# Kernel tuning notes

Measured on AMD Instinct MI355X. Metric: run time of the kernel, lower is better.

The kernel has to match this reference:

```python
import jax, jax.numpy as jnp
import numpy as np

NUM_BINS = 5
TAIL = 1.0
MIN_BIN_W = 1e-3
MIN_BIN_H = 1e-3


def conv2d(x, w, b, pad):
    y = jax.lax.conv_general_dilated(x, w, (1, 1), [(pad, pad), (pad, pad)],
                                     dimension_numbers=("NCHW", "OIHW", "NCHW"))
    return y + b[None, :, None, None]


def transform_net(x, w1, b1, w2, b2, w3, b3):
    h = jax.nn.relu(conv2d(x, w1, b1, 1))
    h = jax.nn.relu(conv2d(h, w2, b2, 0))
    return conv2d(h, w3, b3, 1)


def _pad_last_left(a):
    return jnp.pad(a, [(0, 0)] * (a.ndim - 1) + [(1, 0)])


def quadratic_spline(x, uw, uh):
    # nflows quadratic_spline with left=bottom=-TAIL, right=top=TAIL
    inputs = (x + TAIL) / (2.0 * TAIL)  # rescale to [0,1]
    widths = jax.nn.softmax(uw, axis=-1)
    widths = MIN_BIN_W + (1.0 - MIN_BIN_W * NUM_BINS) * widths
    uh_exp = jnp.exp(uh)  # [..., NUM_BINS-1]
    first_w = 0.5 * widths[..., 0]
    last_w = 0.5 * widths[..., -1]
    numerator = (0.5 * first_w * uh_exp[..., 0] + 0.5 * last_w * uh_exp[..., -1]
                 + jnp.sum(0.5 * (uh_exp[..., :-1] + uh_exp[..., 1:]) * widths[..., 1:-1], axis=-1))
    constant = numerator / (1.0 - 0.5 * first_w - 0.5 * last_w)
    uh_exp = jnp.concatenate([constant[..., None], uh_exp, constant[..., None]], axis=-1)  # NUM_BINS+1 knot heights
    area = jnp.sum(0.5 * (uh_exp[..., :-1] + uh_exp[..., 1:]) * widths, axis=-1, keepdims=True)
    heights = uh_exp / area
    heights = MIN_BIN_H + (1.0 - MIN_BIN_H) * heights
    bin_cdf = jnp.cumsum(0.5 * (heights[..., :-1] + heights[..., 1:]) * widths, axis=-1)
    bin_cdf = _pad_last_left(bin_cdf.at[..., -1].set(1.0))  # [..., NUM_BINS+1]
    bin_loc = jnp.cumsum(widths, axis=-1)
    bin_loc = _pad_last_left(bin_loc.at[..., -1].set(1.0))  # [..., NUM_BINS+1]
    # searchsorted: bin index per element
    idx = jnp.clip(jnp.sum((inputs[..., None] >= bin_loc).astype(jnp.int32), axis=-1) - 1, 0, NUM_BINS - 1)
    take = lambda t, i: jnp.take_along_axis(t, i[..., None], axis=-1)[..., 0]
    loc = take(bin_loc, idx)
    cdf = take(bin_cdf, idx)
    h_l = take(heights, idx)
    h_r = take(heights, idx + 1)
    w = take(widths, idx)
    alpha = (inputs - loc) / w
    a = 0.5 * (h_r - h_l) * w
    b = h_l * w
    out = jnp.clip(a * alpha * alpha + b * alpha + cdf, 0.0, 1.0)
    lad = jnp.log(alpha * (h_r - h_l) + h_l)  # log(top-bottom)-log(right-left)=0
    out = out * (2.0 * TAIL) - TAIL
    return out, lad


def unconstrained_quadratic_spline(x, uw, uh):
    inside = (x >= -TAIL) & (x <= TAIL)
    xc = jnp.clip(x, -TAIL, TAIL)
    s_out, s_lad = quadratic_spline(xc, uw, uh)
    out = jnp.where(inside, s_out, x)  # linear tails
    lad = jnp.where(inside, s_lad, 0.0)
    return out, lad


def setup_inputs() -> dict:
    key = jax.random.key(0)
    ks = jax.random.split(key, 8)
    B, C, H, W = 32, 12, 128, 128
    hid = 128
    c_half = C // 2
    c_out = c_half * (2 * NUM_BINS - 1)  # 54
    s = 0.05
    return {
        "x": jax.random.normal(ks[0], (B, C, H, W), dtype=jnp.float32),
        "objective": jnp.zeros((B,), dtype=jnp.float32),
        "w1": s * jax.random.normal(ks[1], (hid, c_half, 3, 3), dtype=jnp.float32),
        "b1": jnp.zeros((hid,), dtype=jnp.float32),
        "w2": s * jax.random.normal(ks[2], (hid, hid, 1, 1), dtype=jnp.float32),
        "b2": jnp.zeros((hid,), dtype=jnp.float32),
        "w3": s * jax.random.normal(ks[3], (c_out, hid, 3, 3), dtype=jnp.float32),
        "b3": jnp.zeros((c_out,), dtype=jnp.float32),
    }


def reference(x, objective, w1, b1, w2, b2, w3, b3):
    identity_split, transform_split = jnp.split(x, 2, axis=1)
    params = transform_net(identity_split, w1, b1, w2, b2, w3, b3)  # [B, c/2*(2K-1), H, W]
    b, c, h, w = transform_split.shape
    params = params.reshape(b, c, -1, h, w).transpose(0, 1, 3, 4, 2)  # [B,c,H,W,2K-1]
    uw = params[..., :NUM_BINS]
    uh = params[..., NUM_BINS:]
    transformed, lad = unconstrained_quadratic_spline(transform_split, uw, uh)
    output = jnp.concatenate([identity_split, transformed], axis=1)
    objective = objective + jnp.sum(lad, axis=(1, 2, 3))
    return output, objective
```

## Files before the change

### kernel.cpp

```cpp
#include <hip/hip_runtime.h>
#include <hip/hip_bf16.h>
#include <math.h>

#define B 32
#define CFULL 12
#define CH 6
#define HH 128
#define WW 128
#define HID 128
#define CO3 54
#define NB 5
#define OUT_ELEMS (B*CFULL*HH*WW)
#define H2_BYTES (size_t)(B*HH*WW*HID*2)
#define WFRAG_ELEMS (9*4*4*64*8)
#define W1F_ELEMS (2*8*64*8)
#define W2F_ELEMS (4*8*64*8)

typedef __bf16 bf16x8 __attribute__((ext_vector_type(8)));
typedef float f32x4 __attribute__((ext_vector_type(4)));

__device__ __forceinline__ ushort f2bf(float f) {
    uint b = __float_as_uint(f);
    uint r = (b + 0x7FFFu + ((b >> 16) & 1u)) >> 16;
    return (ushort)r;
}

union UBF { uint4 u; bf16x8 b; };

__global__ __launch_bounds__(256) void k_prep_all(
    const float* __restrict__ w1, const float* __restrict__ w2, const float* __restrict__ w3,
    const float* __restrict__ obj_in, float* __restrict__ obj_out,
    ushort* __restrict__ W1f, ushort* __restrict__ W2f, ushort* __restrict__ W3f)
{
    int idx = blockIdx.x * 256 + threadIdx.x;
    if (blockIdx.x == 0 && threadIdx.x < B) obj_out[threadIdx.x] = obj_in[threadIdx.x];

    if (idx < WFRAG_ELEMS) {
        int j    = idx & 7;
        int lane = (idx >> 3) & 63;
        int nf   = (idx >> 9) & 3;
        int kb   = (idx >> 11) & 3;
        int t    = idx >> 13;
        int co = nf * 16 + (lane & 15);
        int ci = kb * 32 + 8 * (lane >> 4) + j;
        float v = (co < CO3) ? w3[(co * HID + ci) * 9 + t] : 0.f;
        W3f[idx] = f2bf(v);
    } else if (idx < WFRAG_ELEMS + W1F_ELEMS) {
        int i1 = idx - WFRAG_ELEMS;
        int j = i1 & 7, lane = (i1 >> 3) & 63, nf = (i1 >> 9) & 7, ks = i1 >> 12;
        int co = nf * 16 + (lane & 15);
        int k  = ks * 32 + (lane >> 4) * 8 + j;
        W1f[i1] = f2bf(k < 54 ? w1[co * 54 + k] : 0.f);
    } else if (idx < WFRAG_ELEMS + W1F_ELEMS + W2F_ELEMS) {
        int i2 = idx - WFRAG_ELEMS - W1F_ELEMS;
        int j = i2 & 7, lane = (i2 >> 3) & 63, nf = (i2 >> 9) & 7, ks = (i2 >> 12) & 3;
        int co = nf * 16 + (lane & 15);
        int ci = ks * 32 + (lane >> 4) * 8 + j;
        W2f[i2] = f2bf(w2[co * 128 + ci]);
    }
}

__global__ __launch_bounds__(256) void k_conv12(
    const float* __restrict__ x,
    const ushort* __restrict__ W1f, const float* __restrict__ b1,
    const ushort* __restrict__ W2f, const float* __restrict__ b2,
    ushort* __restrict__ h2)
{
    __shared__ char buf[32768];

    ushort* xs = (ushort*)buf;
    char* Albase = buf + 4864;
    char* h1 = buf;
    char* h2st = buf;

    const int b = blockIdx.x >> 7;
    const int h = blockIdx.x & 127;
    const int tid = threadIdx.x;
    const int lane = tid & 63;
    const int wv = tid >> 6;
    const int lr = lane & 15;
    const int kg = lane >> 4;

    for (int i = tid; i < 6*3*130; i += 256) {
        int ci = i / 390; int rem = i - ci*390;
        int r = rem / 130; int xw = rem - r*130;
        int hh = h + r - 1, ww = xw - 1;
        float v = 0.f;
        if (hh >= 0 && hh < HH && ww >= 0 && ww < WW)
            v = x[((b*CFULL + ci)*HH + hh)*WW + ww];
        xs[(ci*3 + r)*132 + xw] = f2bf(v);
    }
    __syncthreads();

    for (int it = 0; it < 4; ++it) {
        int item = (it << 8) + tid;
        int px = item & 127;
        int g  = item >> 7;
        uint pk[4];
#pragma unroll
        for (int jj = 0; jj < 4; ++jj) {
            int k0 = g*8 + jj*2;
            int k1 = k0 + 1;
            uint v0 = 0, v1 = 0;
            if (k0 < 54) { int ci = k0/9; int rem = k0 - ci*9; int r = rem/3; int dx = rem - r*3;
                           v0 = xs[(ci*3 + r)*132 + px + dx]; }
            if (k1 < 54) { int ci = k1/9; int rem = k1 - ci*9; int r = rem/3; int dx = rem - r*3;
                           v1 = xs[(ci*3 + r)*132 + px + dx]; }
            pk[jj] = v0 | (v1 << 16);
        }
        uint4 q; q.x = pk[0]; q.y = pk[1]; q.z = pk[2]; q.w = pk[3];
        *(uint4*)(Albase + px*128 + ((g << 4) ^ (((px >> 1) & 7) << 4))) = q;
    }
    __syncthreads();

    f32x4 acc[2][8];
#pragma unroll
    for (int mm = 0; mm < 2; ++mm)
#pragma unroll
        for (int nf = 0; nf < 8; ++nf) acc[mm][nf] = (f32x4){0.f,0.f,0.f,0.f};

    const int px0 = wv*32 + lr;
    const int px1 = px0 + 16;
#pragma unroll
    for (int ks = 0; ks < 2; ++ks) {
        UBF a0, a1;
        a0.u = *(const uint4*)(Albase + px0*128 + ((ks*64 + kg*16) ^ (((px0 >> 1) & 7) << 4)));
        a1.u = *(const uint4*)(Albase + px1*128 + ((ks*64 + kg*16) ^ (((px1 >> 1) & 7) << 4)));
        const char* wp = (const char*)W1f + ks*8192 + lane*16;
#pragma unroll
        for (int nf = 0; nf < 8; ++nf) {
            UBF bf; bf.u = *(const uint4*)(wp + nf*1024);
            acc[0][nf] = __builtin_amdgcn_mfma_f32_16x16x32_bf16(a0.b, bf.b, acc[0][nf], 0, 0, 0);
            acc[1][nf] = __builtin_amdgcn_mfma_f32_16x16x32_bf16(a1.b, bf.b, acc[1][nf], 0, 0, 0);
        }
    }
    __syncthreads();

    float b1v[8];
#pragma unroll
    for (int nf = 0; nf < 8; ++nf) b1v[nf] = b1[nf*16 + lr];
#pragma unroll
    for (int mm = 0; mm < 2; ++mm)
#pragma unroll
        for (int nf = 0; nf < 8; ++nf) {
            int co2 = (nf*16 + lr) * 2;
#pragma unroll
            for (int rg = 0; rg < 4; ++rg) {
                int px = wv*32 + mm*16 + kg*4 + rg;
                float v = fmaxf(acc[mm][nf][rg] + b1v[nf], 0.f);
                *(ushort*)(h1 + px*256 + (co2 ^ (((px >> 1) & 7) << 4))) = f2bf(v);
            }
        }
    __syncthreads();

#pragma unroll
    for (int mm = 0; mm < 2; ++mm)
#pragma unroll
        for (int nf = 0; nf < 8; ++nf) acc[mm][nf] = (f32x4){0.f,0.f,0.f,0.f};
#pragma unroll
    for (int ks = 0; ks < 4; ++ks) {
        UBF a0, a1;
        a0.u = *(const uint4*)(h1 + px0*256 + ((ks*64 + kg*16) ^ (((px0 >> 1) & 7) << 4)));
        a1.u = *(const uint4*)(h1 + px1*256 + ((ks*64 + kg*16) ^ (((px1 >> 1) & 7) << 4)));
        const char* wp = (const char*)W2f + ks*8192 + lane*16;
#pragma unroll
        for (int nf = 0; nf < 8; ++nf) {
            UBF bf; bf.u = *(const uint4*)(wp + nf*1024);
            acc[0][nf] = __builtin_amdgcn_mfma_f32_16x16x32_bf16(a0.b, bf.b, acc[0][nf], 0, 0, 0);
            acc[1][nf] = __builtin_amdgcn_mfma_f32_16x16x32_bf16(a1.b, bf.b, acc[1][nf], 0, 0, 0);
        }
    }
    __syncthreads();

    float b2v[8];
#pragma unroll
    for (int nf = 0; nf < 8; ++nf) b2v[nf] = b2[nf*16 + lr];
#pragma unroll
    for (int mm = 0; mm < 2; ++mm)
#pragma unroll
        for (int nf = 0; nf < 8; ++nf) {
            int co2 = (nf*16 + lr) * 2;
#pragma unroll
            for (int rg = 0; rg < 4; ++rg) {
                int px = wv*32 + mm*16 + kg*4 + rg;
                float v = fmaxf(acc[mm][nf][rg] + b2v[nf], 0.f);
                *(ushort*)(h2st + px*256 + (co2 ^ (((px >> 1) & 7) << 4))) = f2bf(v);
            }
        }
    __syncthreads();

    const size_t outbase = (size_t)((b*HH + h)*WW) * HID;
    for (int c = tid; c < 2048; c += 256) {
        int px = c >> 4; int cb = (c & 15) << 4;
        uint4 v = *(const uint4*)(h2st + px*256 + (cb ^ (((px >> 1) & 7) << 4)));
        *(uint4*)&h2[outbase + (size_t)c*8] = v;
    }
}

__global__ __launch_bounds__(256, 3) void k_conv3_spline(
    const float* __restrict__ x,
    const ushort* __restrict__ h2,
    const ushort* __restrict__ Wfrag, const float* __restrict__ b3,
    float* __restrict__ out, float* __restrict__ obj)
{
    __shared__ char xsb[33792];
    __shared__ float red[4];

    const int g = blockIdx.x;
    const int b = blockIdx.y;
    const int tid = threadIdx.x;
    const int px = tid & 127;
    const int t7 = (tid >> 7) & 1;

    float xr0, xr1, xr2, xr3, xr4, xr5;
    {
        size_t base;
#define PRO(RR, KS, DST) \
        base = ((size_t)(b*CFULL + (t7 + 2*(KS)))*HH + (2*g + (RR)))*WW + px; \
        out[base] = x[base]; \
        DST = x[base + (size_t)CH*HH*WW];
        PRO(0,0,xr0) PRO(0,1,xr1) PRO(0,2,xr2)
        PRO(1,0,xr3) PRO(1,1,xr4) PRO(1,2,xr5)
#undef PRO
    }

    const int lane = tid & 63;
    const int wv   = tid >> 6;
    const int mrow = wv >> 1;
    const int ncol = wv & 1;
    const int kg   = lane >> 4;
    const int lr   = lane & 15;

    f32x4 acc[8][2];
#pragma unroll
    for (int mf = 0; mf < 8; ++mf) {
        acc[mf][0] = (f32x4){0.f,0.f,0.f,0.f};
        acc[mf][1] = (f32x4){0.f,0.f,0.f,0.f};
    }

    const char* wbase = (const char*)Wfrag + ncol*2048 + lane*16;

#pragma unroll 1
    for (int q = 0; q < 4; ++q) {
        if (q) __syncthreads();

        for (int i = tid; i < 2080; i += 256) {
            int r = i / 520; int rem = i - r*520;
            int wl = rem >> 2; int c4 = rem & 3;
            int hh = 2*g - 1 + r, ww = wl - 1;
            uint4 v = {0,0,0,0};
            if (hh >= 0 && hh < HH && ww >= 0 && ww < WW)
                v = *(const uint4*)&h2[(size_t)((b*HH + hh)*WW + ww)*HID + q*32 + c4*8];
            *(uint4*)(xsb + r*8448 + wl*64 + ((c4*16) ^ (((wl >> 1) & 3) << 4))) = v;
        }
        __syncthreads();

#pragma unroll 1
        for (int r3 = 0; r3 < 3; ++r3) {
            const char* rowb = xsb + (mrow + r3)*8448;
#pragma unroll
            for (int dx = 0; dx < 3; ++dx) {
                const int t = r3*3 + dx;
                const char* wp = wbase + (((t << 2) + q) << 12);
                UBF b0; b0.u = *(const uint4*)(wp);
                UBF b1; b1.u = *(const uint4*)(wp + 1024);
#pragma unroll
                for (int mf = 0; mf < 8; ++mf) {
                    const int wl = mf*16 + lr + dx;
                    UBF a; a.u = *(const uint4*)(rowb + wl*64 + ((kg*16) ^ (((wl >> 1) & 3) << 4)));
                    acc[mf][0] = __builtin_amdgcn_mfma_f32_16x16x32_bf16(a.b, b0.b, acc[mf][0], 0, 0, 0);
                    acc[mf][1] = __builtin_amdgcn_mfma_f32_16x16x32_bf16(a.b, b1.b, acc[mf][1], 0, 0, 0);
                }
            }
        }
    }
    __syncthreads();

    float* pl = (float*)xsb;
    float lad = 0.f;

#pragma unroll
    for (int r = 0; r < 2; ++r) {
        if (r) __syncthreads();

        if (mrow == r) {
#pragma unroll
            for (int mf = 0; mf < 8; ++mf)
#pragma unroll
                for (int nf = 0; nf < 2; ++nf) {
                    const int co = ncol*32 + nf*16 + lr;
                    const int p0 = mf*16 + (kg << 2);
                    *(f32x4*)&pl[co*132 + p0] = acc[mf][nf];
                }
        }
        __syncthreads();

#pragma unroll
        for (int ks = 0; ks < 3; ++ks) {
            const int c = __builtin_amdgcn_readfirstlane(t7 + 2*ks);
            const float xraw = (r == 0) ? (ks == 0 ? xr0 : ks == 1 ? xr1 : xr2)
                                        : (ks == 0 ? xr3 : ks == 1 ? xr4 : xr5);

            float u[9];
#pragma unroll
            for (int j = 0; j < 9; ++j) u[j] = pl[(c*9 + j)*132 + px] + b3[c*9 + j];

            bool inside = (xraw >= -1.f) && (xraw <= 1.f);
            float xc = fminf(fmaxf(xraw, -1.f), 1.f);
            float in01 = (xc + 1.f) * 0.5f;

            float m = u[0];
#pragma unroll
            for (int i2 = 1; i2 < 5; ++i2) m = fmaxf(m, u[i2]);
            float e[5], es = 0.f;
#pragma unroll
            for (int i2 = 0; i2 < 5; ++i2) { e[i2] = expf(u[i2] - m); es += e[i2]; }
            float wdt[5];
#pragma unroll
            for (int i2 = 0; i2 < 5; ++i2) wdt[i2] = 0.001f + (1.f - 0.001f*NB) * (e[i2] / es);

            float eh[4];
#pragma unroll
            for (int i2 = 0; i2 < 4; ++i2) eh[i2] = expf(u[5 + i2]);

            float first_w = 0.5f * wdt[0], last_w = 0.5f * wdt[4];
            float numer = 0.5f*first_w*eh[0] + 0.5f*last_w*eh[3]
                        + 0.5f*(eh[0]+eh[1])*wdt[1]
                        + 0.5f*(eh[1]+eh[2])*wdt[2]
                        + 0.5f*(eh[2]+eh[3])*wdt[3];
            float cst = numer / (1.f - 0.5f*first_w - 0.5f*last_w);

            float kn[6] = {cst, eh[0], eh[1], eh[2], eh[3], cst};
            float area = 0.f;
#pragma unroll
            for (int i2 = 0; i2 < 5; ++i2) area += 0.5f*(kn[i2]+kn[i2+1])*wdt[i2];
            float hts[6];
#pragma unroll
            for (int i2 = 0; i2 < 6; ++i2) hts[i2] = 0.001f + (1.f - 0.001f) * (kn[i2] / area);

            float C[6]; C[0] = 0.f;
#pragma unroll
            for (int i2 = 0; i2 < 5; ++i2) C[i2+1] = C[i2] + 0.5f*(hts[i2]+hts[i2+1])*wdt[i2];
            C[5] = 1.f;
            float L[6]; L[0] = 0.f;
#pragma unroll
            for (int i2 = 0; i2 < 5; ++i2) L[i2+1] = L[i2] + wdt[i2];
            L[5] = 1.f;

            int idx = 0;
#pragma unroll
            for (int i2 = 1; i2 < 6; ++i2) idx += (in01 >= L[i2]) ? 1 : 0;
            idx = min(idx, 4);

            float loc = L[0], cdf = C[0], hl = hts[0], hr = hts[1], wb2 = wdt[0];
#pragma unroll
            for (int i2 = 1; i2 < 5; ++i2) {
                if (i2 == idx) { loc = L[i2]; cdf = C[i2]; hl = hts[i2]; hr = hts[i2+1]; wb2 = wdt[i2]; }
            }

            float alpha = (in01 - loc) / wb2;
            float aa = 0.5f*(hr - hl)*wb2;
            float bb = hl*wb2;
            float o = fminf(fmaxf(aa*alpha*alpha + bb*alpha + cdf, 0.f), 1.f);
            float sl = logf(alpha*(hr - hl) + hl);
            float outv = o*2.f - 1.f;
            if (!inside) { outv = xraw; sl = 0.f; }
            out[((size_t)(b*CFULL + CH + c)*HH + (2*g + r))*WW + px] = outv;
            lad += sl;
        }
    }

#pragma unroll
    for (int off = 32; off > 0; off >>= 1) lad += __shfl_down(lad, off, 64);
    if ((tid & 63) == 0) red[tid >> 6] = lad;
    __syncthreads();
    if (tid == 0) {
        float s = red[0] + red[1] + red[2] + red[3];
        atomicAdd(&obj[b], s);
    }
}

extern "C" void kernel_launch(void* const* d_in, const int* in_sizes, int n_in,
                              void* d_out, int out_size, void* d_ws, size_t ws_size,
                              hipStream_t stream) {
    const float* x   = (const float*)d_in[0];
    const float* obj = (const float*)d_in[1];
    const float* w1  = (const float*)d_in[2];
    const float* b1  = (const float*)d_in[3];
    const float* w2  = (const float*)d_in[4];
    const float* b2  = (const float*)d_in[5];
    const float* w3  = (const float*)d_in[6];
    const float* b3  = (const float*)d_in[7];

    float* out_t = (float*)d_out;
    float* obj_o = out_t + OUT_ELEMS;
    ushort* h2  = (ushort*)d_ws;
    ushort* W3f = (ushort*)((char*)d_ws + H2_BYTES);
    ushort* W1f = (ushort*)((char*)d_ws + H2_BYTES + 147456);
    ushort* W2f = (ushort*)((char*)d_ws + H2_BYTES + 147456 + 16384);

    const int prep_items = WFRAG_ELEMS + W1F_ELEMS + W2F_ELEMS;
    k_prep_all<<<(prep_items + 255)/256, 256, 0, stream>>>(w1, w2, w3, obj, obj_o, W1f, W2f, W3f);
    k_conv12<<<B*HH, 256, 0, stream>>>(x, W1f, b1, W2f, b2, h2);
    k_conv3_spline<<<dim3(HH/2, B), 256, 0, stream>>>(x, h2, W3f, b3, out_t, obj_o);
}
```

Measured before the change: 278.1 us.

## Prefetch next conv3 channel slab into registers and vectorize conv1/conv2 epilogue stores

In the conv3+spline kernel, the global loads of the next 32-channel h2 slab are issued into registers before the MFMA loop over the current slab and written to LDS afterwards, so global latency overlaps with compute. In the conv1/conv2 kernel, the MFMA operands are swapped so each lane holds four consecutive output channels for one pixel. The epilogue then packs them into a single 8-byte LDS store with a float4 bias load, replacing four scalar 2-byte stores. The prefetch costs 9 uint4 registers per thread (36 VGPRs), which may pressure occupancy under launch_bounds(256,3).

New measurement: 391.1 us. +40.6%, slower.

```diff
diff --git a/kernel.cpp b/kernel.cpp
--- a/kernel.cpp
+++ b/kernel.cpp
@@ -23,6 +23,9 @@
     uint b = __float_as_uint(f);
     uint r = (b + 0x7FFFu + ((b >> 16) & 1u)) >> 16;
     return (ushort)r;
+}
+__device__ __forceinline__ uint pack2(float a, float b) {
+    return (uint)f2bf(a) | ((uint)f2bf(b) << 16);
 }
 
 union UBF { uint4 u; bf16x8 b; };
@@ -130,27 +133,28 @@
 #pragma unroll
         for (int nf = 0; nf < 8; ++nf) {
             UBF bf; bf.u = *(const uint4*)(wp + nf*1024);
-            acc[0][nf] = __builtin_amdgcn_mfma_f32_16x16x32_bf16(a0.b, bf.b, acc[0][nf], 0, 0, 0);
-            acc[1][nf] = __builtin_amdgcn_mfma_f32_16x16x32_bf16(a1.b, bf.b, acc[1][nf], 0, 0, 0);
-        }
-    }
-    __syncthreads();
-
-    float b1v[8];
-#pragma unroll
-    for (int nf = 0; nf < 8; ++nf) b1v[nf] = b1[nf*16 + lr];
-#pragma unroll
-    for (int mm = 0; mm < 2; ++mm)
+            acc[0][nf] = __builtin_amdgcn_mfma_f32_16x16x32_bf16(bf.b, a0.b, acc[0][nf], 0, 0, 0);
+            acc[1][nf] = __builtin_amdgcn_mfma_f32_16x16x32_bf16(bf.b, a1.b, acc[1][nf], 0, 0, 0);
+        }
+    }
+    __syncthreads();
+
+#pragma unroll
+    for (int mm = 0; mm < 2; ++mm) {
+        const int pxm = wv*32 + mm*16 + lr;
+        const int swz = ((pxm >> 1) & 7) << 4;
 #pragma unroll
         for (int nf = 0; nf < 8; ++nf) {
-            int co2 = (nf*16 + lr) * 2;
-#pragma unroll
-            for (int rg = 0; rg < 4; ++rg) {
-                int px = wv*32 + mm*16 + kg*4 + rg;
-                float v = fmaxf(acc[mm][nf][rg] + b1v[nf], 0.f);
-                *(ushort*)(h1 + px*256 + (co2 ^ (((px >> 1) & 7) << 4))) = f2bf(v);
-            }
-        }
+            const int co0 = nf*16 + kg*4;
+            float4 bb = *(const float4*)&b1[co0];
+            float v0 = fmaxf(acc[mm][nf][0] + bb.x, 0.f);
+            float v1 = fmaxf(acc[mm][nf][1] + bb.y, 0.f);
+            float v2 = fmaxf(acc[mm][nf][2] + bb.z, 0.f);
+            float v3 = fmaxf(acc[mm][nf][3] + bb.w, 0.f);
+            uint2 p; p.x = pack2(v0, v1); p.y = pack2(v2, v3);
+            *(uint2*)(h1 + pxm*256 + ((co0*2) ^ swz)) = p;
+        }
+    }
     __syncthreads();
 
 #pragma unroll
@@ -166,27 +170,28 @@
 #pragma unroll
         for (int nf = 0; nf < 8; ++nf) {
             UBF bf; bf.u = *(const uint4*)(wp + nf*1024);
-            acc[0][nf] = __builtin_amdgcn_mfma_f32_16x16x32_bf16(a0.b, bf.b, acc[0][nf], 0, 0, 0);
-            acc[1][nf] = __builtin_amdgcn_mfma_f32_16x16x32_bf16(a1.b, bf.b, acc[1][nf], 0, 0, 0);
-        }
-    }
-    __syncthreads();
-
-    float b2v[8];
-#pragma unroll
-    for (int nf = 0; nf < 8; ++nf) b2v[nf] = b2[nf*16 + lr];
-#pragma unroll
-    for (int mm = 0; mm < 2; ++mm)
+            acc[0][nf] = __builtin_amdgcn_mfma_f32_16x16x32_bf16(bf.b, a0.b, acc[0][nf], 0, 0, 0);
+            acc[1][nf] = __builtin_amdgcn_mfma_f32_16x16x32_bf16(bf.b, a1.b, acc[1][nf], 0, 0, 0);
+        }
+    }
+    __syncthreads();
+
+#pragma unroll
+    for (int mm = 0; mm < 2; ++mm) {
+        const int pxm = wv*32 + mm*16 + lr;
+        const int swz = ((pxm >> 1) & 7) << 4;
 #pragma unroll
         for (int nf = 0; nf < 8; ++nf) {
-            int co2 = (nf*16 + lr) * 2;
-#pragma unroll
-            for (int rg = 0; rg < 4; ++rg) {
-                int px = wv*32 + mm*16 + kg*4 + rg;
-                float v = fmaxf(acc[mm][nf][rg] + b2v[nf], 0.f);
-                *(ushort*)(h2st + px*256 + (co2 ^ (((px >> 1) & 7) << 4))) = f2bf(v);
-            }
-        }
+            const int co0 = nf*16 + kg*4;
+            float4 bb = *(const float4*)&b2[co0];
+            float v0 = fmaxf(acc[mm][nf][0] + bb.x, 0.f);
+            float v1 = fmaxf(acc[mm][nf][1] + bb.y, 0.f);
+            float v2 = fmaxf(acc[mm][nf][2] + bb.z, 0.f);
+            float v3 = fmaxf(acc[mm][nf][3] + bb.w, 0.f);
+            uint2 p; p.x = pack2(v0, v1); p.y = pack2(v2, v3);
+            *(uint2*)(h2st + pxm*256 + ((co0*2) ^ swz)) = p;
+        }
+    }
     __syncthreads();
 
     const size_t outbase = (size_t)((b*HH + h)*WW) * HID;
@@ -240,20 +245,41 @@
 
     const char* wbase = (const char*)Wfrag + ncol*2048 + lane*16;
 
+    uint4 vq[9];
+
+#define STAGE_LOAD(Q) \
+    _Pragma("unroll") \
+    for (int k = 0; k < 9; ++k) { \
+        int i = tid + (k << 8); \
+        if (i < 2080) { \
+            int r = i / 520; int rem = i - r*520; \
+            int wl = rem >> 2; int c4 = rem & 3; \
+            int hh = 2*g - 1 + r, ww = wl - 1; \
+            uint4 v = {0,0,0,0}; \
+            if (hh >= 0 && hh < HH && ww >= 0 && ww < WW) \
+                v = *(const uint4*)&h2[(size_t)((b*HH + hh)*WW + ww)*HID + (Q)*32 + c4*8]; \
+            vq[k] = v; \
+        } \
+    }
+
+#define STAGE_WRITE() \
+    _Pragma("unroll") \
+    for (int k = 0; k < 9; ++k) { \
+        int i = tid + (k << 8); \
+        if (i < 2080) { \
+            int r = i / 520; int rem = i - r*520; \
+            int wl = rem >> 2; int c4 = rem & 3; \
+            *(uint4*)(xsb + r*8448 + wl*64 + ((c4*16) ^ (((wl >> 1) & 3) << 4))) = vq[k]; \
+        } \
+    }
+
+    STAGE_LOAD(0);
+    STAGE_WRITE();
+    __syncthreads();
+
 #pragma unroll 1
     for (int q = 0; q < 4; ++q) {
-        if (q) __syncthreads();
-
-        for (int i = tid; i < 2080; i += 256) {
-            int r = i / 520; int rem = i - r*520;
-            int wl = rem >> 2; int c4 = rem & 3;
-            int hh = 2*g - 1 + r, ww = wl - 1;
-            uint4 v = {0,0,0,0};
-            if (hh >= 0 && hh < HH && ww >= 0 && ww < WW)
-                v = *(const uint4*)&h2[(size_t)((b*HH + hh)*WW + ww)*HID + q*32 + c4*8];
-            *(uint4*)(xsb + r*8448 + wl*64 + ((c4*16) ^ (((wl >> 1) & 3) << 4))) = v;
-        }
-        __syncthreads();
+        if (q < 3) STAGE_LOAD(q + 1);
 
 #pragma unroll 1
         for (int r3 = 0; r3 < 3; ++r3) {
@@ -273,8 +299,13 @@
                 }
             }
         }
-    }
-    __syncthreads();
+
+        __syncthreads();
+        if (q < 3) {
+            STAGE_WRITE();
+            __syncthreads();
+        }
+    }
 
     float* pl = (float*)xsb;
     float lad = 0.f;
@@ -378,6 +409,8 @@
         float s = red[0] + red[1] + red[2] + red[3];
         atomicAdd(&obj[b], s);
     }
+#undef STAGE_LOAD
+#undef STAGE_WRITE
 }
 
 extern "C" void kernel_launch(void* const* d_in, const int* in_sizes, int n_in,
```
